# Optimization experiments

Hardware: AMD Instinct MI355X
Metric: run time of the kernel (lower is better)

Reference implementation:

```python
import jax, jax.numpy as jnp
import numpy as np

M = 128      # molecules
L = 256      # max nodes per molecule (padding length)
H = 768      # hidden_size
NH = 12      # num_heads
HD = H // NH # head_dim
N = M * L    # total flat nodes
EPS = 1e-5


def setup_inputs() -> dict:
    key = jax.random.key(0)
    ks = jax.random.split(key, 12)
    s = 1.0 / np.sqrt(H)
    atom_features = jax.random.normal(ks[0], (N, H), dtype=jnp.float32)
    a_starts = jnp.arange(M, dtype=jnp.int32) * L
    a_sizes = jax.random.randint(ks[1], (M,), L // 2, L + 1, dtype=jnp.int32)
    inp = {
        'atom_features': atom_features,
        'Wq': jax.random.normal(ks[2], (H, H), jnp.float32) * s,
        'bq': jnp.zeros((H,), jnp.float32),
        'Wk': jax.random.normal(ks[3], (H, H), jnp.float32) * s,
        'bk': jnp.zeros((H,), jnp.float32),
        'Wv': jax.random.normal(ks[4], (H, H), jnp.float32) * s,
        'bv': jnp.zeros((H,), jnp.float32),
        'Wo': jax.random.normal(ks[5], (H, H), jnp.float32) * s,
        'bo': jnp.zeros((H,), jnp.float32),
        'gamma': jnp.ones((H,), jnp.float32),
        'beta': jnp.zeros((H,), jnp.float32),
        'a_starts': a_starts,
        'a_sizes': a_sizes,
    }
    return inp


def reference(atom_features, Wq, bq, Wk, bk, Wv, bv, Wo, bo, gamma, beta,
              a_starts, a_sizes):
    scale = HD ** -0.5
    pos = jnp.arange(L, dtype=jnp.int32)
    idx = a_starts[:, None] + pos[None, :]                      # [M, L]
    mask = pos[None, :] < a_sizes[:, None]                      # [M, L] valid nodes
    x = atom_features[idx] * mask[..., None]                    # [M, L, H]

    def proj(W, b):
        y = jnp.einsum('mlh,oh->mlo', x, W) + b                 # torch Linear: x @ W.T + b
        return y.reshape(M, L, NH, HD).transpose(0, 2, 1, 3)    # [M, NH, L, HD]

    q, k, v = proj(Wq, bq), proj(Wk, bk), proj(Wv, bv)
    scores = jnp.einsum('mhqd,mhkd->mhqk', q, k) * scale        # [M, NH, L, L]
    scores = jnp.where(mask[:, None, None, :], scores, -1e9)
    attn = jax.nn.softmax(scores, axis=-1)
    ctx = jnp.einsum('mhqk,mhkd->mhqd', attn, v)                # [M, NH, L, HD]
    ctx = ctx.transpose(0, 2, 1, 3).reshape(M, L, H)
    out = jnp.einsum('mlh,oh->mlo', ctx, Wo) + bo

    y = out + x                                                 # residual
    mu = jnp.mean(y, axis=-1, keepdims=True)
    var = jnp.mean((y - mu) ** 2, axis=-1, keepdims=True)
    y = (y - mu) * jax.lax.rsqrt(var + EPS) * gamma + beta
    y = y * mask[..., None]

    enhanced = jnp.zeros_like(atom_features).at[idx.reshape(-1)].set(
        y.reshape(-1, H))
    return enhanced
```

## Files before the change

kernel.cpp:

```cpp
#include <hip/hip_runtime.h>
#include <hip/hip_bf16.h>
#include <stdint.h>

#define M_MOL 128
#define L_SEQ 256
#define H_DIM 768
#define NH_   12
#define HD_   64
#define N_TOT (M_MOL * L_SEQ)

typedef __attribute__((ext_vector_type(8))) short bf16x8;
typedef __attribute__((ext_vector_type(4))) float f32x4;
typedef __attribute__((ext_vector_type(8))) unsigned short u16x8;
typedef __hip_bfloat16 bf16;

__device__ __forceinline__ float bf2f(bf16 x){ return __bfloat162float(x); }
__device__ __forceinline__ bf16 f2bf(float x){ return __float2bfloat16(x); }
__device__ __forceinline__ float bfbits2f(unsigned short u){
    return __uint_as_float(((unsigned)u) << 16);
}
__device__ __forceinline__ unsigned pk2(float lo, float hi){
    bf16 a = f2bf(lo), b = f2bf(hi);
    unsigned short ua, ub;
    __builtin_memcpy(&ua, &a, 2);
    __builtin_memcpy(&ub, &b, 2);
    return (unsigned)ua | ((unsigned)ub << 16);
}

typedef const __attribute__((address_space(1))) unsigned int* as1_u32p;
typedef __attribute__((address_space(3))) unsigned int* as3_u32p;
__device__ __forceinline__ void async_ld16(const void* g, const void* l) {
    __builtin_amdgcn_global_load_lds((as1_u32p)(unsigned long long)g,
                                     (as3_u32p)(unsigned int)(unsigned long long)l,
                                     16, 0, 0);
}

#define MFMA16(a,b,c) __builtin_amdgcn_mfma_f32_16x16x32_bf16((a),(b),(c),0,0,0)

__global__ __launch_bounds__(256)
void cvt_all(const float* __restrict__ af, const float* __restrict__ Wq,
             const float* __restrict__ Wk, const float* __restrict__ Wv,
             const float* __restrict__ Wo,
             bf16* __restrict__ afb, bf16* __restrict__ Wcat, bf16* __restrict__ Wobf)
{
    const int b = blockIdx.x;
    const float* src; bf16* dst; int local;
    if (b < 12288) { src = af; dst = afb; local = b; }
    else {
        int r = b - 12288;
        int mat = r / 288; local = r % 288;
        src = mat==0 ? Wq : mat==1 ? Wk : mat==2 ? Wv : Wo;
        dst = (mat < 3) ? (Wcat + (size_t)mat*589824) : Wobf;
    }
    const size_t off = ((size_t)local*256 + threadIdx.x)*8;
    float4 a = *(const float4*)(src + off);
    float4 c = *(const float4*)(src + off + 4);
    uint4 o = { pk2(a.x,a.y), pk2(a.z,a.w), pk2(c.x,c.y), pk2(c.z,c.w) };
    *(uint4*)(dst + off) = o;
}

__device__ __forceinline__ void gemm256_core(
    const bf16* __restrict__ Ap, const bf16* __restrict__ Wp,
    int rowBase, int colBase, char* sm, f32x4 (&acc)[8][4])
{
    const int t = threadIdx.x;
    const int w = t >> 6, lane = t & 63, quad = lane >> 4, r16 = lane & 15;
    const int wr = w >> 2, wc = w & 3;
    const int r0  = t >> 3;
    const int kbe = (((t & 7) ^ (r0 & 7)) << 3);
    const int aBase = (wr*128 + r16) * 128;
    const int bBase = 32768 + (wc*64 + r16) * 128;
    const int swz = (r16 & 7) << 4;
    const int cs0 = (0  + quad*16) ^ swz;
    const int cs1 = (64 + quad*16) ^ swz;

#pragma unroll
    for (int i = 0; i < 8; ++i)
#pragma unroll
        for (int j = 0; j < 4; ++j) acc[i][j] = (f32x4){0.f,0.f,0.f,0.f};

    auto stage = [&](int isB, int T, int h) {
        const bf16* g = isB ? Wp : Ap;
        const int gr0 = (isB ? colBase : rowBase) + h*128 + r0;
        const bf16* p0 = g + (size_t)gr0*768 + T*64 + kbe;
        char* reg = sm + ((T&1)*65536 + isB*32768 + h*16384 + w*1024);
        async_ld16(p0, reg);
        async_ld16(p0 + (size_t)64*768, reg + 8192);
    };

    stage(0,0,0); stage(0,0,1);
    stage(1,0,0); stage(1,0,1);
    stage(0,1,0); stage(0,1,1);
    asm volatile("s_waitcnt vmcnt(4)" ::: "memory");
    __builtin_amdgcn_s_barrier();

    bf16x8 a0[4][2], a1[4][2], b0v[2][2], b1v[2][2];

    for (int T = 0; T < 12; ++T) {
        const char* Bf = sm + (T&1)*65536;

        if (T+1 < 12) { stage(1, T+1, 0); stage(1, T+1, 1); }
#pragma unroll
        for (int mi = 0; mi < 4; ++mi) {
            a0[mi][0] = *(const bf16x8*)(Bf + aBase + mi*2048 + cs0);
            a0[mi][1] = *(const bf16x8*)(Bf + aBase + mi*2048 + cs1);
        }
#pragma unroll
        for (int ni = 0; ni < 2; ++ni) {
            b0v[ni][0] = *(const bf16x8*)(Bf + bBase + ni*2048 + cs0);
            b0v[ni][1] = *(const bf16x8*)(Bf + bBase + ni*2048 + cs1);
        }
#pragma unroll
        for (int mi = 0; mi < 4; ++mi) {
            a1[mi][0] = *(const bf16x8*)(Bf + aBase + 8192 + mi*2048 + cs0);
            a1[mi][1] = *(const bf16x8*)(Bf + aBase + 8192 + mi*2048 + cs1);
        }
        __builtin_amdgcn_s_setprio(1);
#pragma unroll
        for (int mi = 0; mi < 4; ++mi)
#pragma unroll
            for (int ni = 0; ni < 2; ++ni) {
                acc[mi][ni] = MFMA16(a0[mi][0], b0v[ni][0], acc[mi][ni]);
                acc[mi][ni] = MFMA16(a0[mi][1], b0v[ni][1], acc[mi][ni]);
            }
        __builtin_amdgcn_s_setprio(0);
#pragma unroll
        for (int ni = 0; ni < 2; ++ni) {
            b1v[ni][0] = *(const bf16x8*)(Bf + bBase + 4096 + ni*2048 + cs0);
            b1v[ni][1] = *(const bf16x8*)(Bf + bBase + 4096 + ni*2048 + cs1);
        }
        __builtin_amdgcn_s_setprio(1);
#pragma unroll
        for (int mi = 0; mi < 4; ++mi)
#pragma unroll
            for (int ni = 0; ni < 2; ++ni) {
                acc[4+mi][ni] = MFMA16(a1[mi][0], b0v[ni][0], acc[4+mi][ni]);
                acc[4+mi][ni] = MFMA16(a1[mi][1], b0v[ni][1], acc[4+mi][ni]);
            }
        __builtin_amdgcn_s_setprio(0);
        asm volatile("s_waitcnt lgkmcnt(0)" ::: "memory");
        __builtin_amdgcn_sched_barrier(0);
        __builtin_amdgcn_s_barrier();

        if (T+2 < 12) { stage(0, T+2, 0); stage(0, T+2, 1); }
        __builtin_amdgcn_s_setprio(1);
#pragma unroll
        for (int mi = 0; mi < 4; ++mi)
#pragma unroll
            for (int ni = 0; ni < 2; ++ni) {
                acc[mi][2+ni] = MFMA16(a0[mi][0], b1v[ni][0], acc[mi][2+ni]);
                acc[mi][2+ni] = MFMA16(a0[mi][1], b1v[ni][1], acc[mi][2+ni]);
            }
#pragma unroll
        for (int mi = 0; mi < 4; ++mi)
#pragma unroll
            for (int ni = 0; ni < 2; ++ni) {
                acc[4+mi][2+ni] = MFMA16(a1[mi][0], b1v[ni][0], acc[4+mi][2+ni]);
                acc[4+mi][2+ni] = MFMA16(a1[mi][1], b1v[ni][1], acc[4+mi][2+ni]);
            }
        __builtin_amdgcn_s_setprio(0);
        if (T < 10)       { asm volatile("s_waitcnt vmcnt(4)" ::: "memory"); }
        else if (T == 10) { asm volatile("s_waitcnt vmcnt(0)" ::: "memory"); }
        if (T < 11) __builtin_amdgcn_s_barrier();
    }
}

__global__ __launch_bounds__(512, 2)
void gemm_qkv(const bf16* __restrict__ A, const bf16* __restrict__ W,
              const float* __restrict__ bq, const float* __restrict__ bk,
              const float* __restrict__ bv,
              bf16* __restrict__ qb, bf16* __restrict__ kb, bf16* __restrict__ vb)
{
    __shared__ __align__(16) char sm[131072];
    const int bid = blockIdx.x;
    const int xcd = bid & 7, idx = bid >> 3;
    const int rowBlk = xcd*16 + idx/9;
    const int colBlk = idx - (idx/9)*9;
    const int rowBase = rowBlk * 256;
    const int colBase = colBlk * 256;

    f32x4 acc[8][4];
    gemm256_core(A, W, rowBase, colBase, sm, acc);

    const int t = threadIdx.x;
    const int w = t >> 6, lane = t & 63, quad = lane >> 4, r16 = lane & 15;
    const int wr = w >> 2, wc = w & 3;
    const int sel = colBlk / 3;
    const float* bias = sel==0 ? bq : sel==1 ? bk : bv;
    bf16* C = sel==0 ? qb : sel==1 ? kb : vb;
    const int colSec = colBase - sel*768;
#pragma unroll
    for (int nj = 0; nj < 4; ++nj) {
        int col = colSec + wc*64 + nj*16 + r16;
        float bb = bias[col];
#pragma unroll
        for (int mi = 0; mi < 8; ++mi) {
            int row0 = rowBase + wr*128 + mi*16 + quad*4;
#pragma unroll
            for (int rr = 0; rr < 4; ++rr)
                C[(size_t)(row0+rr)*768 + col] = f2bf(acc[mi][nj][rr] + bb);
        }
    }
}

__global__ __launch_bounds__(512, 2)
void gemm_o(const bf16* __restrict__ A, const bf16* __restrict__ W,
            const float* __restrict__ bo, bf16* __restrict__ C)
{
    __shared__ __align__(16) char sm[131072];
    const int bid = blockIdx.x;
    const int xcd = bid & 7, idx = bid >> 3;
    const int rowBlk = xcd*16 + idx/3;
    const int colBlk = idx - (idx/3)*3;
    const int rowBase = rowBlk * 256;
    const int colBase = colBlk * 256;

    f32x4 acc[8][4];
    gemm256_core(A, W, rowBase, colBase, sm, acc);

    const int t = threadIdx.x;
    const int w = t >> 6, lane = t & 63, quad = lane >> 4, r16 = lane & 15;
    const int wr = w >> 2, wc = w & 3;
#pragma unroll
    for (int nj = 0; nj < 4; ++nj) {
        int col = colBase + wc*64 + nj*16 + r16;
        float bb = bo[col];
#pragma unroll
        for (int mi = 0; mi < 8; ++mi) {
            int row0 = rowBase + wr*128 + mi*16 + quad*4;
#pragma unroll
            for (int rr = 0; rr < 4; ++rr)
                C[(size_t)(row0+rr)*768 + col] = f2bf(acc[mi][nj][rr] + bb);
        }
    }
}

__global__ __launch_bounds__(256, 2)
void attn_kernel(const bf16* __restrict__ qbuf, const bf16* __restrict__ kbuf,
                 bf16* vctx, const int* __restrict__ a_sizes)
{
    __shared__ __align__(16) bf16 VT[64*264];
    __shared__ __align__(16) bf16 P[4*16*264];

    const int b = blockIdx.x;
    const int m = b / NH_, nh = b % NH_;
    const int t = threadIdx.x;
    const int w = t >> 6, lane = t & 63, quad = lane >> 4, r16 = lane & 15;
    const int size = a_sizes[m];
    const size_t headOff = (size_t)m*L_SEQ*768 + nh*64;

    {
        const int k0 = (t & 127) * 2;
        const int dh = (t >> 7) * 32;
        const bf16* v0 = vctx + headOff + (size_t)k0*768 + dh;
        const bf16* v1 = v0 + 768;
        u16x8 r0[4], r1[4];
#pragma unroll
        for (int c = 0; c < 4; ++c) {
            r0[c] = *(const u16x8*)(v0 + c*8);
            r1[c] = *(const u16x8*)(v1 + c*8);
        }
#pragma unroll
        for (int c = 0; c < 4; ++c)
#pragma unroll
            for (int j = 0; j < 8; ++j) {
                unsigned val = (unsigned)r0[c][j] | ((unsigned)r1[c][j] << 16);
                *(unsigned*)(&VT[(size_t)(dh + c*8 + j)*264 + k0]) = val;
            }
    }
    __syncthreads();

    bf16x8 kf0[16], kf1[16];
#pragma unroll
    for (int kt = 0; kt < 16; ++kt) {
        const bf16* krow = kbuf + headOff + (size_t)(kt*16 + r16)*768 + quad*8;
        kf0[kt] = *(const bf16x8*)(krow);
        kf1[kt] = *(const bf16x8*)(krow + 32);
    }

    bf16* Pw = P + w*16*264;
    for (int pass = 0; pass < 4; ++pass) {
        const int qrow0 = pass*64 + w*16;
        bf16x8 aq0, aq1;
        {
            const bf16* qrow = qbuf + headOff + (size_t)(qrow0 + r16)*768 + quad*8;
            aq0 = *(const bf16x8*)(qrow);
            aq1 = *(const bf16x8*)(qrow + 32);
        }
        f32x4 S[16];
#pragma unroll
        for (int kt = 0; kt < 16; ++kt) {
            f32x4 s = (f32x4){0.f,0.f,0.f,0.f};
            s = __builtin_amdgcn_mfma_f32_16x16x32_bf16(aq0, kf0[kt], s, 0, 0, 0);
            s = __builtin_amdgcn_mfma_f32_16x16x32_bf16(aq1, kf1[kt], s, 0, 0, 0);
            S[kt] = s;
        }
        float mrow[4] = {-1e30f,-1e30f,-1e30f,-1e30f};
#pragma unroll
        for (int kt = 0; kt < 16; ++kt) {
            int key = kt*16 + r16;
#pragma unroll
            for (int rr = 0; rr < 4; ++rr) {
                float s = S[kt][rr] * 0.125f;
                if (key >= size) s = -1e9f;
                S[kt][rr] = s;
                mrow[rr] = fmaxf(mrow[rr], s);
            }
        }
#pragma unroll
        for (int msk = 1; msk < 16; msk <<= 1)
#pragma unroll
            for (int rr = 0; rr < 4; ++rr)
                mrow[rr] = fmaxf(mrow[rr], __shfl_xor(mrow[rr], msk));
        float lrow[4] = {0.f,0.f,0.f,0.f};
#pragma unroll
        for (int kt = 0; kt < 16; ++kt) {
#pragma unroll
            for (int rr = 0; rr < 4; ++rr) {
                float p = __expf(S[kt][rr] - mrow[rr]);
                lrow[rr] += p;
                Pw[(quad*4+rr)*264 + kt*16 + r16] = f2bf(p);
            }
        }
#pragma unroll
        for (int msk = 1; msk < 16; msk <<= 1)
#pragma unroll
            for (int rr = 0; rr < 4; ++rr)
                lrow[rr] += __shfl_xor(lrow[rr], msk);
        asm volatile("s_waitcnt lgkmcnt(0)" ::: "memory");

        bf16x8 pa[8];
#pragma unroll
        for (int kb2 = 0; kb2 < 8; ++kb2)
            pa[kb2] = *(const bf16x8*)(&Pw[r16*264 + kb2*32 + quad*8]);
        float inv[4];
#pragma unroll
        for (int rr = 0; rr < 4; ++rr) inv[rr] = 1.f / lrow[rr];
#pragma unroll
        for (int dt = 0; dt < 4; ++dt) {
            f32x4 c = (f32x4){0.f,0.f,0.f,0.f};
#pragma unroll
            for (int kb2 = 0; kb2 < 8; ++kb2) {
                bf16x8 vb8 = *(const bf16x8*)(&VT[(dt*16 + r16)*264 + kb2*32 + quad*8]);
                c = __builtin_amdgcn_mfma_f32_16x16x32_bf16(pa[kb2], vb8, c, 0, 0, 0);
            }
#pragma unroll
            for (int rr = 0; rr < 4; ++rr) {
                int q = qrow0 + quad*4 + rr;
                vctx[headOff + (size_t)q*768 + dt*16 + r16] = f2bf(c[rr] * inv[rr]);
            }
        }
    }
}

__global__ __launch_bounds__(256, 4)
void ln_kernel(const bf16* __restrict__ proj, const float* __restrict__ af,
               const float* __restrict__ gamma, const float* __restrict__ beta,
               const int* __restrict__ a_sizes, float* __restrict__ out)
{
    const int w = threadIdx.x >> 6, lane = threadIdx.x & 63;
    const int n = blockIdx.x * 4 + w;
    const int m = n >> 8, l = n & 255;
    const int size = a_sizes[m];
    float* orow = out + (size_t)n * 768;
    if (l >= size) {
        float4 z = {0.f,0.f,0.f,0.f};
#pragma unroll
        for (int i = 0; i < 3; ++i) *(float4*)(&orow[i*256 + lane*4]) = z;
        return;
    }
    const bf16*  prow = proj + (size_t)n * 768;
    const float* xrow = af   + (size_t)n * 768;
    float y[3][4];
    float s = 0.f;
#pragma unroll
    for (int i = 0; i < 3; ++i) {
        int c = i*256 + lane*4;
        float4 xv = *(const float4*)(&xrow[c]);
        ushort4 pv = *(const ushort4*)(&prow[c]);
        y[i][0] = xv.x + bfbits2f(pv.x);
        y[i][1] = xv.y + bfbits2f(pv.y);
        y[i][2] = xv.z + bfbits2f(pv.z);
        y[i][3] = xv.w + bfbits2f(pv.w);
        s += y[i][0] + y[i][1] + y[i][2] + y[i][3];
    }
#pragma unroll
    for (int msk = 1; msk < 64; msk <<= 1) s += __shfl_xor(s, msk);
    float mu = s * (1.f/768.f);
    float v = 0.f;
#pragma unroll
    for (int i = 0; i < 3; ++i)
#pragma unroll
        for (int j = 0; j < 4; ++j) { float d = y[i][j] - mu; v += d*d; }
#pragma unroll
    for (int msk = 1; msk < 64; msk <<= 1) v += __shfl_xor(v, msk);
    float rstd = rsqrtf(v * (1.f/768.f) + 1e-5f);
#pragma unroll
    for (int i = 0; i < 3; ++i) {
        int c = i*256 + lane*4;
        float4 gv = *(const float4*)(&gamma[c]);
        float4 bv = *(const float4*)(&beta[c]);
        float4 o;
        o.x = (y[i][0] - mu) * rstd * gv.x + bv.x;
        o.y = (y[i][1] - mu) * rstd * gv.y + bv.y;
        o.z = (y[i][2] - mu) * rstd * gv.z + bv.z;
        o.w = (y[i][3] - mu) * rstd * gv.w + bv.w;
        *(float4*)(&orow[c]) = o;
    }
}

extern "C" void kernel_launch(void* const* d_in, const int* in_sizes, int n_in,
                              void* d_out, int out_size, void* d_ws, size_t ws_size,
                              hipStream_t stream)
{
    (void)in_sizes; (void)n_in; (void)out_size; (void)ws_size;
    const float* af    = (const float*)d_in[0];
    const float* Wq    = (const float*)d_in[1];
    const float* bq    = (const float*)d_in[2];
    const float* Wk    = (const float*)d_in[3];
    const float* bk    = (const float*)d_in[4];
    const float* Wv    = (const float*)d_in[5];
    const float* bv    = (const float*)d_in[6];
    const float* Wo    = (const float*)d_in[7];
    const float* bo    = (const float*)d_in[8];
    const float* gamma = (const float*)d_in[9];
    const float* beta  = (const float*)d_in[10];
    const int* a_sizes = (const int*)d_in[12];
    float* outp = (float*)d_out;

    bf16* qb = (bf16*)d_ws;
    bf16* kb = qb + (size_t)N_TOT * 768;
    bf16* vb = kb + (size_t)N_TOT * 768;
    bf16* afb  = (bf16*)d_out;
    bf16* Wcat = afb + (size_t)N_TOT * 768;
    bf16* Wobf = Wcat + (size_t)2304 * 768;

    cvt_all<<<dim3(12288 + 4*288), 256, 0, stream>>>(af, Wq, Wk, Wv, Wo, afb, Wcat, Wobf);
    gemm_qkv<<<dim3(1152), 512, 0, stream>>>(afb, Wcat, bq, bk, bv, qb, kb, vb);
    attn_kernel<<<dim3(M_MOL * NH_), 256, 0, stream>>>(qb, kb, vb, a_sizes);
    gemm_o<<<dim3(384), 512, 0, stream>>>(vb, Wobf, bo, qb);
    ln_kernel<<<dim3(N_TOT / 4), 256, 0, stream>>>(qb, af, gamma, beta, a_sizes, outp);
}
```

Measured before the change: 489.7 us.

## Load GEMM B operand directly from global into registers, stage only A in LDS

Reworks the shared GEMM core so the weight (B) tile is read straight from global memory into registers each K-step, and only the activation (A) tile is staged through LDS with async loads. The K tile is doubled to 128, so there are 6 iterations instead of 12, with a new XOR swizzle for the A layout. The aim is to cut LDS traffic and barrier work for B and to make each iteration larger. In exchange, B loads are not prefetched, so global/L2 latency sits on the critical path, and B is read redundantly by the two wave rows.

```diff
diff --git a/kernel.cpp b/kernel.cpp
--- a/kernel.cpp
+++ b/kernel.cpp
@@ -66,102 +66,74 @@
     const int t = threadIdx.x;
     const int w = t >> 6, lane = t & 63, quad = lane >> 4, r16 = lane & 15;
     const int wr = w >> 2, wc = w & 3;
-    const int r0  = t >> 3;
-    const int kbe = (((t & 7) ^ (r0 & 7)) << 3);
-    const int aBase = (wr*128 + r16) * 128;
-    const int bBase = 32768 + (wc*64 + r16) * 128;
-    const int swz = (r16 & 7) << 4;
-    const int cs0 = (0  + quad*16) ^ swz;
-    const int cs1 = (64 + quad*16) ^ swz;
+
+    const int sr = w*4 + quad;
+    const int gk = ((r16 ^ (sr & 7)) << 3);
+    const int aswz  = r16 & 7;
+    const int arowB = (wr*128 + r16) * 256;
+
+    const bf16* brow0 = Wp + (size_t)(colBase + wc*64 +  0 + r16)*768 + quad*8;
+    const bf16* brow1 = Wp + (size_t)(colBase + wc*64 + 16 + r16)*768 + quad*8;
+    const bf16* brow2 = Wp + (size_t)(colBase + wc*64 + 32 + r16)*768 + quad*8;
+    const bf16* brow3 = Wp + (size_t)(colBase + wc*64 + 48 + r16)*768 + quad*8;
 
 #pragma unroll
     for (int i = 0; i < 8; ++i)
 #pragma unroll
         for (int j = 0; j < 4; ++j) acc[i][j] = (f32x4){0.f,0.f,0.f,0.f};
 
-    auto stage = [&](int isB, int T, int h) {
-        const bf16* g = isB ? Wp : Ap;
-        const int gr0 = (isB ? colBase : rowBase) + h*128 + r0;
-        const bf16* p0 = g + (size_t)gr0*768 + T*64 + kbe;
-        char* reg = sm + ((T&1)*65536 + isB*32768 + h*16384 + w*1024);
-        async_ld16(p0, reg);
-        async_ld16(p0 + (size_t)64*768, reg + 8192);
+    auto stageA = [&](int T) {
+        char* base = sm + (T&1)*65536 + w*1024;
+        const bf16* g = Ap + (size_t)(rowBase + sr)*768 + T*128 + gk;
+#pragma unroll
+        for (int p = 0; p < 8; ++p)
+            async_ld16(g + (size_t)p*32*768, base + p*8192);
     };
 
-    stage(0,0,0); stage(0,0,1);
-    stage(1,0,0); stage(1,0,1);
-    stage(0,1,0); stage(0,1,1);
-    asm volatile("s_waitcnt vmcnt(4)" ::: "memory");
+    stageA(0); stageA(1);
+    asm volatile("s_waitcnt vmcnt(8)" ::: "memory");
     __builtin_amdgcn_s_barrier();
 
-    bf16x8 a0[4][2], a1[4][2], b0v[2][2], b1v[2][2];
-
-    for (int T = 0; T < 12; ++T) {
+    for (int T = 0; T < 6; ++T) {
         const char* Bf = sm + (T&1)*65536;
-
-        if (T+1 < 12) { stage(1, T+1, 0); stage(1, T+1, 1); }
-#pragma unroll
-        for (int mi = 0; mi < 4; ++mi) {
-            a0[mi][0] = *(const bf16x8*)(Bf + aBase + mi*2048 + cs0);
-            a0[mi][1] = *(const bf16x8*)(Bf + aBase + mi*2048 + cs1);
-        }
-#pragma unroll
-        for (int ni = 0; ni < 2; ++ni) {
-            b0v[ni][0] = *(const bf16x8*)(Bf + bBase + ni*2048 + cs0);
-            b0v[ni][1] = *(const bf16x8*)(Bf + bBase + ni*2048 + cs1);
-        }
-#pragma unroll
-        for (int mi = 0; mi < 4; ++mi) {
-            a1[mi][0] = *(const bf16x8*)(Bf + aBase + 8192 + mi*2048 + cs0);
-            a1[mi][1] = *(const bf16x8*)(Bf + aBase + 8192 + mi*2048 + cs1);
-        }
-        __builtin_amdgcn_s_setprio(1);
-#pragma unroll
-        for (int mi = 0; mi < 4; ++mi)
-#pragma unroll
-            for (int ni = 0; ni < 2; ++ni) {
-                acc[mi][ni] = MFMA16(a0[mi][0], b0v[ni][0], acc[mi][ni]);
-                acc[mi][ni] = MFMA16(a0[mi][1], b0v[ni][1], acc[mi][ni]);
-            }
-        __builtin_amdgcn_s_setprio(0);
-#pragma unroll
-        for (int ni = 0; ni < 2; ++ni) {
-            b1v[ni][0] = *(const bf16x8*)(Bf + bBase + 4096 + ni*2048 + cs0);
-            b1v[ni][1] = *(const bf16x8*)(Bf + bBase + 4096 + ni*2048 + cs1);
-        }
-        __builtin_amdgcn_s_setprio(1);
-#pragma unroll
-        for (int mi = 0; mi < 4; ++mi)
-#pragma unroll
-            for (int ni = 0; ni < 2; ++ni) {
-                acc[4+mi][ni] = MFMA16(a1[mi][0], b0v[ni][0], acc[4+mi][ni]);
-                acc[4+mi][ni] = MFMA16(a1[mi][1], b0v[ni][1], acc[4+mi][ni]);
-            }
-        __builtin_amdgcn_s_setprio(0);
+        const int tOff = T*128;
+
+        bf16x8 b[4][4];
+#pragma unroll
+        for (int kk = 0; kk < 4; ++kk) {
+            b[kk][0] = *(const bf16x8*)(brow0 + tOff + kk*32);
+            b[kk][1] = *(const bf16x8*)(brow1 + tOff + kk*32);
+            b[kk][2] = *(const bf16x8*)(brow2 + tOff + kk*32);
+            b[kk][3] = *(const bf16x8*)(brow3 + tOff + kk*32);
+        }
+
+#pragma unroll
+        for (int kk = 0; kk < 4; ++kk) {
+            bf16x8 a0[8];
+#pragma unroll
+            for (int mi = 0; mi < 8; ++mi)
+                a0[mi] = *(const bf16x8*)(Bf + arowB + mi*4096 +
+                                          (((kk*4 + quad) ^ aswz) << 4));
+            __builtin_amdgcn_s_setprio(1);
+#pragma unroll
+            for (int mi = 0; mi < 8; ++mi)
+#pragma unroll
+                for (int ni = 0; ni < 4; ++ni)
+                    acc[mi][ni] = MFMA16(a0[mi], b[kk][ni], acc[mi][ni]);
+            __builtin_amdgcn_s_setprio(0);
+        }
+
         asm volatile("s_waitcnt lgkmcnt(0)" ::: "memory");
         __builtin_amdgcn_sched_barrier(0);
         __builtin_amdgcn_s_barrier();
 
-        if (T+2 < 12) { stage(0, T+2, 0); stage(0, T+2, 1); }
-        __builtin_amdgcn_s_setprio(1);
-#pragma unroll
-        for (int mi = 0; mi < 4; ++mi)
-#pragma unroll
-            for (int ni = 0; ni < 2; ++ni) {
-                acc[mi][2+ni] = MFMA16(a0[mi][0], b1v[ni][0], acc[mi][2+ni]);
-                acc[mi][2+ni] = MFMA16(a0[mi][1], b1v[ni][1], acc[mi][2+ni]);
-            }
-#pragma unroll
-        for (int mi = 0; mi < 4; ++mi)
-#pragma unroll
-            for (int ni = 0; ni < 2; ++ni) {
-                acc[4+mi][2+ni] = MFMA16(a1[mi][0], b1v[ni][0], acc[4+mi][2+ni]);
-                acc[4+mi][2+ni] = MFMA16(a1[mi][1], b1v[ni][1], acc[4+mi][2+ni]);
-            }
-        __builtin_amdgcn_s_setprio(0);
-        if (T < 10)       { asm volatile("s_waitcnt vmcnt(4)" ::: "memory"); }
-        else if (T == 10) { asm volatile("s_waitcnt vmcnt(0)" ::: "memory"); }
-        if (T < 11) __builtin_amdgcn_s_barrier();
+        if (T+2 < 6) {
+            stageA(T+2);
+            asm volatile("s_waitcnt vmcnt(8)" ::: "memory");
+        } else if (T == 4) {
+            asm volatile("s_waitcnt vmcnt(0)" ::: "memory");
+        }
+        if (T < 5) __builtin_amdgcn_s_barrier();
     }
 }
 
```

Measured after the change: 585.9 us. 1.2x slower.

## Fuse fp32-to-bf16 activation conversion into QKV GEMM A-tile loading

Applied to the files above, without the earlier changes.

Removes the separate conversion pass over atom_features. The QKV GEMM now reads fp32 activations into registers, converts them to bf16 and writes them to LDS itself, while weights are still converted by a smaller kernel. This saves writing and re-reading a bf16 copy of the activations. In exchange the A operand is read at fp32 width, 9 times across the column blocks, and goes through registers instead of async global-to-LDS loads. The prefetch is shallower (one tile ahead, full vmcnt(0) waits), so loads may be less well hidden.

```diff
diff --git a/kernel.cpp b/kernel.cpp
--- a/kernel.cpp
+++ b/kernel.cpp
@@ -38,20 +38,14 @@
 #define MFMA16(a,b,c) __builtin_amdgcn_mfma_f32_16x16x32_bf16((a),(b),(c),0,0,0)
 
 __global__ __launch_bounds__(256)
-void cvt_all(const float* __restrict__ af, const float* __restrict__ Wq,
-             const float* __restrict__ Wk, const float* __restrict__ Wv,
-             const float* __restrict__ Wo,
-             bf16* __restrict__ afb, bf16* __restrict__ Wcat, bf16* __restrict__ Wobf)
-{
-    const int b = blockIdx.x;
-    const float* src; bf16* dst; int local;
-    if (b < 12288) { src = af; dst = afb; local = b; }
-    else {
-        int r = b - 12288;
-        int mat = r / 288; local = r % 288;
-        src = mat==0 ? Wq : mat==1 ? Wk : mat==2 ? Wv : Wo;
-        dst = (mat < 3) ? (Wcat + (size_t)mat*589824) : Wobf;
-    }
+void cvt_w(const float* __restrict__ Wq, const float* __restrict__ Wk,
+           const float* __restrict__ Wv, const float* __restrict__ Wo,
+           bf16* __restrict__ Wcat, bf16* __restrict__ Wobf)
+{
+    const int r = blockIdx.x;
+    const int mat = r / 288, local = r % 288;
+    const float* src = mat==0 ? Wq : mat==1 ? Wk : mat==2 ? Wv : Wo;
+    bf16* dst = (mat < 3) ? (Wcat + (size_t)mat*589824) : Wobf;
     const size_t off = ((size_t)local*256 + threadIdx.x)*8;
     float4 a = *(const float4*)(src + off);
     float4 c = *(const float4*)(src + off + 4);
@@ -59,15 +53,20 @@
     *(uint4*)(dst + off) = o;
 }
 
+template<bool AF32>
 __device__ __forceinline__ void gemm256_core(
-    const bf16* __restrict__ Ap, const bf16* __restrict__ Wp,
+    const void* __restrict__ Avp, const bf16* __restrict__ Wp,
     int rowBase, int colBase, char* sm, f32x4 (&acc)[8][4])
 {
+    const bf16*  Ab = (const bf16*)Avp;
+    const float* Af = (const float*)Avp;
     const int t = threadIdx.x;
     const int w = t >> 6, lane = t & 63, quad = lane >> 4, r16 = lane & 15;
     const int wr = w >> 2, wc = w & 3;
     const int r0  = t >> 3;
     const int kbe = (((t & 7) ^ (r0 & 7)) << 3);
+    const int fcol   = (t & 7) * 8;
+    const int wslot0 = ((t & 7) ^ (r0 & 7)) << 4;
     const int aBase = (wr*128 + r16) * 128;
     const int bBase = 32768 + (wc*64 + r16) * 128;
     const int swz = (r16 & 7) << 4;
@@ -79,49 +78,86 @@
 #pragma unroll
         for (int j = 0; j < 4; ++j) acc[i][j] = (f32x4){0.f,0.f,0.f,0.f};
 
-    auto stage = [&](int isB, int T, int h) {
-        const bf16* g = isB ? Wp : Ap;
+    auto stageG = [&](int isB, int T, int h) {
+        const bf16* g = isB ? Wp : Ab;
         const int gr0 = (isB ? colBase : rowBase) + h*128 + r0;
         const bf16* p0 = g + (size_t)gr0*768 + T*64 + kbe;
-        char* reg = sm + ((T&1)*65536 + isB*32768 + h*16384 + w*1024);
-        async_ld16(p0, reg);
-        async_ld16(p0 + (size_t)64*768, reg + 8192);
+        char* dst = sm + ((T&1)*65536 + isB*32768 + h*16384 + w*1024);
+        async_ld16(p0, dst);
+        async_ld16(p0 + (size_t)64*768, dst + 8192);
     };
 
-    stage(0,0,0); stage(0,0,1);
-    stage(1,0,0); stage(1,0,1);
-    stage(0,1,0); stage(0,1,1);
-    asm volatile("s_waitcnt vmcnt(4)" ::: "memory");
-    __builtin_amdgcn_s_barrier();
-
-    bf16x8 a0[4][2], a1[4][2], b0v[2][2], b1v[2][2];
+    float4 a00,a01,a10,a11,a20,a21,a30,a31;
+    auto loadA = [&](int T){
+        const float* pa = Af + (size_t)(rowBase + r0)*768 + T*64 + fcol;
+        a00 = *(const float4*)(pa);             a01 = *(const float4*)(pa + 4);
+        a10 = *(const float4*)(pa +  64*768);   a11 = *(const float4*)(pa +  64*768 + 4);
+        a20 = *(const float4*)(pa + 128*768);   a21 = *(const float4*)(pa + 128*768 + 4);
+        a30 = *(const float4*)(pa + 192*768);   a31 = *(const float4*)(pa + 192*768 + 4);
+    };
+    auto writeA = [&](int T){
+        char* ab = sm + (T&1)*65536;
+        uint4 o0 = { pk2(a00.x,a00.y), pk2(a00.z,a00.w), pk2(a01.x,a01.y), pk2(a01.z,a01.w) };
+        uint4 o1 = { pk2(a10.x,a10.y), pk2(a10.z,a10.w), pk2(a11.x,a11.y), pk2(a11.z,a11.w) };
+        uint4 o2 = { pk2(a20.x,a20.y), pk2(a20.z,a20.w), pk2(a21.x,a21.y), pk2(a21.z,a21.w) };
+        uint4 o3 = { pk2(a30.x,a30.y), pk2(a30.z,a30.w), pk2(a31.x,a31.y), pk2(a31.z,a31.w) };
+        *(uint4*)(ab + (r0      )*128 + wslot0) = o0;
+        *(uint4*)(ab + (r0 +  64)*128 + wslot0) = o1;
+        *(uint4*)(ab + (r0 + 128)*128 + wslot0) = o2;
+        *(uint4*)(ab + (r0 + 192)*128 + wslot0) = o3;
+    };
+
+    if constexpr (AF32) {
+        loadA(0);
+        stageG(1,0,0); stageG(1,0,1);
+        writeA(0);
+        asm volatile("s_waitcnt vmcnt(0) lgkmcnt(0)" ::: "memory");
+        __builtin_amdgcn_s_barrier();
+    } else {
+        stageG(0,0,0); stageG(0,0,1); stageG(1,0,0); stageG(1,0,1);
+        stageG(0,1,0); stageG(0,1,1);
+        asm volatile("s_waitcnt vmcnt(4)" ::: "memory");
+        __builtin_amdgcn_s_barrier();
+    }
+
+    bf16x8 fa0[4][2], fa1[4][2], b0v[2][2], b1v[2][2];
 
     for (int T = 0; T < 12; ++T) {
         const char* Bf = sm + (T&1)*65536;
 
-        if (T+1 < 12) { stage(1, T+1, 0); stage(1, T+1, 1); }
+        if (AF32 && T+1 < 12) loadA(T+1);
+        if (T+1 < 12) { stageG(1, T+1, 0); stageG(1, T+1, 1); }
 #pragma unroll
         for (int mi = 0; mi < 4; ++mi) {
-            a0[mi][0] = *(const bf16x8*)(Bf + aBase + mi*2048 + cs0);
-            a0[mi][1] = *(const bf16x8*)(Bf + aBase + mi*2048 + cs1);
+            fa0[mi][0] = *(const bf16x8*)(Bf + aBase + mi*2048 + cs0);
+            fa0[mi][1] = *(const bf16x8*)(Bf + aBase + mi*2048 + cs1);
         }
 #pragma unroll
         for (int ni = 0; ni < 2; ++ni) {
             b0v[ni][0] = *(const bf16x8*)(Bf + bBase + ni*2048 + cs0);
             b0v[ni][1] = *(const bf16x8*)(Bf + bBase + ni*2048 + cs1);
         }
+        __builtin_amdgcn_s_setprio(1);
+#pragma unroll
+        for (int mi = 0; mi < 4; ++mi)
+#pragma unroll
+            for (int ni = 0; ni < 2; ++ni) {
+                acc[mi][ni] = MFMA16(fa0[mi][0], b0v[ni][0], acc[mi][ni]);
+                acc[mi][ni] = MFMA16(fa0[mi][1], b0v[ni][1], acc[mi][ni]);
+            }
+        __builtin_amdgcn_s_setprio(0);
 #pragma unroll
         for (int mi = 0; mi < 4; ++mi) {
-            a1[mi][0] = *(const bf16x8*)(Bf + aBase + 8192 + mi*2048 + cs0);
-            a1[mi][1] = *(const bf16x8*)(Bf + aBase + 8192 + mi*2048 + cs1);
+            fa1[mi][0] = *(const bf16x8*)(Bf + aBase + 8192 + mi*2048 + cs0);
+            fa1[mi][1] = *(const bf16x8*)(Bf + aBase + 8192 + mi*2048 + cs1);
         }
         __builtin_amdgcn_s_setprio(1);
 #pragma unroll
         for (int mi = 0; mi < 4; ++mi)
 #pragma unroll
             for (int ni = 0; ni < 2; ++ni) {
-                acc[mi][ni] = MFMA16(a0[mi][0], b0v[ni][0], acc[mi][ni]);
-                acc[mi][ni] = MFMA16(a0[mi][1], b0v[ni][1], acc[mi][ni]);
+                acc[4+mi][ni] = MFMA16(fa1[mi][0], b0v[ni][0], acc[4+mi][ni]);
+                acc[4+mi][ni] = MFMA16(fa1[mi][1], b0v[ni][1], acc[4+mi][ni]);
             }
         __builtin_amdgcn_s_setprio(0);
 #pragma unroll
@@ -129,44 +165,44 @@
             b1v[ni][0] = *(const bf16x8*)(Bf + bBase + 4096 + ni*2048 + cs0);
             b1v[ni][1] = *(const bf16x8*)(Bf + bBase + 4096 + ni*2048 + cs1);
         }
-        __builtin_amdgcn_s_setprio(1);
-#pragma unroll
-        for (int mi = 0; mi < 4; ++mi)
-#pragma unroll
-            for (int ni = 0; ni < 2; ++ni) {
-                acc[4+mi][ni] = MFMA16(a1[mi][0], b0v[ni][0], acc[4+mi][ni]);
-                acc[4+mi][ni] = MFMA16(a1[mi][1], b0v[ni][1], acc[4+mi][ni]);
-            }
-        __builtin_amdgcn_s_setprio(0);
         asm volatile("s_waitcnt lgkmcnt(0)" ::: "memory");
         __builtin_amdgcn_sched_barrier(0);
         __builtin_amdgcn_s_barrier();
 
-        if (T+2 < 12) { stage(0, T+2, 0); stage(0, T+2, 1); }
+        if constexpr (AF32) {
+            if (T+1 < 12) writeA(T+1);
+        } else {
+            if (T+2 < 12) { stageG(0, T+2, 0); stageG(0, T+2, 1); }
+        }
         __builtin_amdgcn_s_setprio(1);
 #pragma unroll
         for (int mi = 0; mi < 4; ++mi)
 #pragma unroll
             for (int ni = 0; ni < 2; ++ni) {
-                acc[mi][2+ni] = MFMA16(a0[mi][0], b1v[ni][0], acc[mi][2+ni]);
-                acc[mi][2+ni] = MFMA16(a0[mi][1], b1v[ni][1], acc[mi][2+ni]);
+                acc[mi][2+ni] = MFMA16(fa0[mi][0], b1v[ni][0], acc[mi][2+ni]);
+                acc[mi][2+ni] = MFMA16(fa0[mi][1], b1v[ni][1], acc[mi][2+ni]);
             }
 #pragma unroll
         for (int mi = 0; mi < 4; ++mi)
 #pragma unroll
             for (int ni = 0; ni < 2; ++ni) {
-                acc[4+mi][2+ni] = MFMA16(a1[mi][0], b1v[ni][0], acc[4+mi][2+ni]);
-                acc[4+mi][2+ni] = MFMA16(a1[mi][1], b1v[ni][1], acc[4+mi][2+ni]);
+                acc[4+mi][2+ni] = MFMA16(fa1[mi][0], b1v[ni][0], acc[4+mi][2+ni]);
+                acc[4+mi][2+ni] = MFMA16(fa1[mi][1], b1v[ni][1], acc[4+mi][2+ni]);
             }
         __builtin_amdgcn_s_setprio(0);
-        if (T < 10)       { asm volatile("s_waitcnt vmcnt(4)" ::: "memory"); }
-        else if (T == 10) { asm volatile("s_waitcnt vmcnt(0)" ::: "memory"); }
+        if constexpr (AF32) {
+            asm volatile("s_waitcnt lgkmcnt(0)" ::: "memory");
+            if (T+1 < 12) { asm volatile("s_waitcnt vmcnt(0)" ::: "memory"); }
+        } else {
+            if (T < 10)       { asm volatile("s_waitcnt vmcnt(4)" ::: "memory"); }
+            else if (T == 10) { asm volatile("s_waitcnt vmcnt(0)" ::: "memory"); }
+        }
         if (T < 11) __builtin_amdgcn_s_barrier();
     }
 }
 
 __global__ __launch_bounds__(512, 2)
-void gemm_qkv(const bf16* __restrict__ A, const bf16* __restrict__ W,
+void gemm_qkv(const float* __restrict__ A, const bf16* __restrict__ W,
               const float* __restrict__ bq, const float* __restrict__ bk,
               const float* __restrict__ bv,
               bf16* __restrict__ qb, bf16* __restrict__ kb, bf16* __restrict__ vb)
@@ -180,7 +216,7 @@
     const int colBase = colBlk * 256;
 
     f32x4 acc[8][4];
-    gemm256_core(A, W, rowBase, colBase, sm, acc);
+    gemm256_core<true>(A, W, rowBase, colBase, sm, acc);
 
     const int t = threadIdx.x;
     const int w = t >> 6, lane = t & 63, quad = lane >> 4, r16 = lane & 15;
@@ -216,7 +252,7 @@
     const int colBase = colBlk * 256;
 
     f32x4 acc[8][4];
-    gemm256_core(A, W, rowBase, colBase, sm, acc);
+    gemm256_core<false>(A, W, rowBase, colBase, sm, acc);
 
     const int t = threadIdx.x;
     const int w = t >> 6, lane = t & 63, quad = lane >> 4, r16 = lane & 15;
@@ -431,12 +467,11 @@
     bf16* qb = (bf16*)d_ws;
     bf16* kb = qb + (size_t)N_TOT * 768;
     bf16* vb = kb + (size_t)N_TOT * 768;
-    bf16* afb  = (bf16*)d_out;
-    bf16* Wcat = afb + (size_t)N_TOT * 768;
+    bf16* Wcat = (bf16*)d_out;
     bf16* Wobf = Wcat + (size_t)2304 * 768;
 
-    cvt_all<<<dim3(12288 + 4*288), 256, 0, stream>>>(af, Wq, Wk, Wv, Wo, afb, Wcat, Wobf);
-    gemm_qkv<<<dim3(1152), 512, 0, stream>>>(afb, Wcat, bq, bk, bv, qb, kb, vb);
+    cvt_w<<<dim3(4*288), 256, 0, stream>>>(Wq, Wk, Wv, Wo, Wcat, Wobf);
+    gemm_qkv<<<dim3(1152), 512, 0, stream>>>(af, Wcat, bq, bk, bv, qb, kb, vb);
     attn_kernel<<<dim3(M_MOL * NH_), 256, 0, stream>>>(qb, kb, vb, a_sizes);
     gemm_o<<<dim3(384), 512, 0, stream>>>(vb, Wobf, bo, qb);
     ln_kernel<<<dim3(N_TOT / 4), 256, 0, stream>>>(qb, af, gamma, beta, a_sizes, outp);
```

After: 549.7 us. +12.2%, slower.
